# Kernel tuning notes

Measured on AMD Instinct MI355X. Metric: run time of the kernel, lower is better.

## Reference

```python
import jax, jax.numpy as jnp
import numpy as np

B, T, D, H = 4, 2048, 1024, 16
HD = D // H  # 64


def setup_inputs() -> dict:
    key = jax.random.key(0)
    k1, k2, k3 = jax.random.split(key, 3)
    x = jax.random.normal(k1, (B, T, D), dtype=jnp.float32)
    # xavier-uniform-ish scaling for stability
    W_qkv = jax.random.normal(k2, (3 * D, D), dtype=jnp.float32) * (1.0 / np.sqrt(D))
    W_proj = jax.random.normal(k3, (D, D), dtype=jnp.float32) * (1.0 / np.sqrt(D))
    b_proj = jnp.zeros((D,), dtype=jnp.float32)
    return {"x": x, "W_qkv": W_qkv, "W_proj": W_proj, "b_proj": b_proj}


def reference(x, W_qkv, W_proj, b_proj):
    Bx, Tx, C = x.shape
    qkv = x @ W_qkv.T                      # [B,T,3C]
    q, k, v = jnp.split(qkv, 3, axis=-1)
    # [B,T,C] -> [B,H,T,hd]
    def heads(t):
        return t.reshape(Bx, Tx, H, HD).transpose(0, 2, 1, 3)
    q, k, v = heads(q), heads(k), heads(v)
    scale = 1.0 / np.sqrt(HD)
    scores = jnp.einsum('bhqd,bhkd->bhqk', q, k) * scale  # [B,H,T,T]
    causal = jnp.tril(jnp.ones((Tx, Tx), dtype=bool))
    scores = jnp.where(causal, scores, jnp.finfo(scores.dtype).min)
    attn = jax.nn.softmax(scores, axis=-1)
    out = jnp.einsum('bhqk,bhkd->bhqd', attn, v)          # [B,H,T,hd]
    out = out.transpose(0, 2, 1, 3).reshape(Bx, Tx, C)    # [B,T,C]
    return out @ W_proj.T + b_proj
```

## Files before the change

kernel.cpp:

```cpp
#include <hip/hip_runtime.h>
#include <hip/hip_bf16.h>

#define B_  4
#define T_  2048
#define D_  1024
#define H_  16
#define HD_ 64
#define THREE_D (3 * D_)
#define TWO_D   (2 * D_)

typedef short s16x8 __attribute__((ext_vector_type(8)));
typedef float f32x4 __attribute__((ext_vector_type(4)));
typedef unsigned short u16;
typedef unsigned short u16x4 __attribute__((ext_vector_type(4)));
typedef unsigned int u32x2 __attribute__((ext_vector_type(2)));

static __device__ __forceinline__ s16x8 load8(const u16* p) {
    return *reinterpret_cast<const s16x8*>(p);
}
static __device__ __forceinline__ u16 f2bf(float f) {
    __hip_bfloat16 h = __float2bfloat16(f);
    return *reinterpret_cast<u16*>(&h);
}
static __device__ __forceinline__ unsigned pktrunc(float lo, float hi) {
#if __has_builtin(__builtin_amdgcn_perm)
    return __builtin_amdgcn_perm(__builtin_bit_cast(unsigned, hi),
                                 __builtin_bit_cast(unsigned, lo),
                                 0x07060302u);
#else
    return (__builtin_bit_cast(unsigned, hi) & 0xFFFF0000u) |
           (__builtin_bit_cast(unsigned, lo) >> 16);
#endif
}
static __device__ __forceinline__ float fast_exp2(float x) {
#if __has_builtin(__builtin_amdgcn_exp2f)
    return __builtin_amdgcn_exp2f(x);
#else
    float r;
    asm("v_exp_f32 %0, %1" : "=v"(r) : "v"(x));
    return r;
#endif
}

static __device__ __forceinline__ void gload_lds16(const u16* g, u16* l) {
#if __has_builtin(__builtin_amdgcn_global_load_lds)
    __builtin_amdgcn_global_load_lds(
        (__attribute__((address_space(1))) void*)g,
        (__attribute__((address_space(3))) void*)l, 16, 0, 0);
#else
    *reinterpret_cast<s16x8*>(l) = load8(g);
#endif
}

__global__ __launch_bounds__(256) void cvt3_f32_bf16(
    const float* __restrict__ a, u16* __restrict__ oa, int na,
    const float* __restrict__ bsrc, u16* __restrict__ ob, int nb,
    const float* __restrict__ c, u16* __restrict__ oc, int nc)
{
    int i = (blockIdx.x * 256 + threadIdx.x) * 4;
    const float* s; u16* d;
    if (i < na)                { s = a;    d = oa; }
    else if ((i -= na) < nb)   { s = bsrc; d = ob; }
    else if ((i -= nb) < nc)   { s = c;    d = oc; }
    else return;
    const float4 f = *reinterpret_cast<const float4*>(s + i);
    u16x4 r;
    r.x = f2bf(f.x); r.y = f2bf(f.y); r.z = f2bf(f.z); r.w = f2bf(f.w);
    *reinterpret_cast<u16x4*>(d + i) = r;
}

template<int MODE>
__global__ __launch_bounds__(256) void gemm_bt128(
    const u16* __restrict__ A,
    const u16* __restrict__ Bm,
    void* __restrict__ Cv,
    const float* __restrict__ bias,
    int M, int N, int K, int lda, int ldb, int ldc,
    float qsc, u16* __restrict__ vt)
{
    const int ntiles = N >> 7;
    const int nwg  = (M >> 7) * ntiles;
    const int cpx  = nwg >> 3;
    const int mtpc = cpx / ntiles;
    const int xcd  = (int)blockIdx.x & 7;
    const int lc   = (int)blockIdx.x >> 3;
    const int nt = lc / mtpc;
    const int mt = xcd * mtpc + (lc % mtpc);
    const int m0 = mt * 128, n0 = nt * 128;
    const int tid  = threadIdx.x;
    const int lane = tid & 63;
    const int l15  = lane & 15;
    const int quad = lane >> 4;
    const int wave = tid >> 6;
    const int wm = (wave >> 1) * 64;
    const int wn = (wave & 1) * 64;

    __shared__ u16 A_sh[2][128 * 32];
    __shared__ u16 B_sh[2][128 * 32];

    f32x4 acc[4][4] = {};

    const int c0 = tid, c1 = tid + 256;
    const int ar0 = c0 >> 2, as0 = (((c0 & 3) ^ ((c0 >> 3) & 3)) * 8);
    const int ar1 = c1 >> 2, as1 = (((c1 & 3) ^ ((c1 >> 3) & 3)) * 8);
    const u16* Ag0 = A  + (size_t)(m0 + ar0) * lda + as0;
    const u16* Ag1 = A  + (size_t)(m0 + ar1) * lda + as1;
    const u16* Bg0 = Bm + (size_t)(n0 + ar0) * ldb + as0;
    const u16* Bg1 = Bm + (size_t)(n0 + ar1) * ldb + as1;

    const int rsw2 = (l15 >> 1) & 3;
    const int rdo  = ((quad ^ rsw2) * 8);

    for (int k0 = 0; k0 < K; k0 += 64) {
        __syncthreads();
        #pragma unroll
        for (int p = 0; p < 2; ++p) {
            gload_lds16(Ag0 + k0 + p * 32, &A_sh[p][c0 * 8]);
            gload_lds16(Ag1 + k0 + p * 32, &A_sh[p][c1 * 8]);
            gload_lds16(Bg0 + k0 + p * 32, &B_sh[p][c0 * 8]);
            gload_lds16(Bg1 + k0 + p * 32, &B_sh[p][c1 * 8]);
        }
        __syncthreads();

        #pragma unroll
        for (int p = 0; p < 2; ++p) {
            s16x8 a[4], b[4];
            #pragma unroll
            for (int i = 0; i < 4; ++i) {
                a[i] = *reinterpret_cast<const s16x8*>(&A_sh[p][(wm + i * 16 + l15) * 32 + rdo]);
                b[i] = *reinterpret_cast<const s16x8*>(&B_sh[p][(wn + i * 16 + l15) * 32 + rdo]);
            }
            #pragma unroll
            for (int mi = 0; mi < 4; ++mi)
                #pragma unroll
                for (int ni = 0; ni < 4; ++ni)
                    acc[mi][ni] = __builtin_amdgcn_mfma_f32_16x16x32_bf16(
                        a[mi], b[ni], acc[mi][ni], 0, 0, 0);
        }
    }

    #pragma unroll
    for (int ni = 0; ni < 4; ++ni) {
        const int col = n0 + wn + ni * 16 + l15;
        if (MODE == 0) {
            const float bv = bias ? bias[col] : 0.0f;
            #pragma unroll
            for (int mi = 0; mi < 4; ++mi) {
                const int row = m0 + wm + mi * 16 + quad * 4;
                #pragma unroll
                for (int r = 0; r < 4; ++r)
                    ((float*)Cv)[(size_t)(row + r) * ldc + col] = acc[mi][ni][r] + bv;
            }
        } else {
            if (col < TWO_D) {
                const float sc = (col < D_) ? qsc : 1.0f;
                #pragma unroll
                for (int mi = 0; mi < 4; ++mi) {
                    const int row = m0 + wm + mi * 16 + quad * 4;
                    #pragma unroll
                    for (int r = 0; r < 4; ++r)
                        ((u16*)Cv)[(size_t)(row + r) * ldc + col] = f2bf(acc[mi][ni][r] * sc);
                }
            } else {
                const int vc = col - TWO_D;
                #pragma unroll
                for (int mi = 0; mi < 4; ++mi) {
                    const int row = m0 + wm + mi * 16 + quad * 4;
                    const int bb = row >> 11, t = row & (T_ - 1);
                    u16x4 pk;
                    #pragma unroll
                    for (int r = 0; r < 4; ++r) pk[r] = f2bf(acc[mi][ni][r]);
                    *reinterpret_cast<u16x4*>(
                        vt + ((size_t)(bb * H_ * HD_) + vc) * T_ + t) = pk;
                }
            }
        }
    }
}

__global__ __launch_bounds__(256) void flash_attn6x(
    const u16* __restrict__ qk, const u16* __restrict__ vt,
    u16* __restrict__ out)
{
    const int cls = blockIdx.x >> 6;
    const int bh  = blockIdx.x & 63;
    const int qmap[16] = {15,14,13,12, 8,9,10,11, 7,6,5,4, 0,1,2,3};
    const int qt = qmap[cls];
    const int h = bh & 15, b = bh >> 4;
    const int q0 = qt * 128;

    __shared__ u16 K_lds[64 * 64];
    __shared__ u16 V_lds[64 * 64];
    __shared__ u16 P_lds[4 * 32 * 72];

    const int tid = threadIdx.x;
    const int wave = tid >> 6, lane = tid & 63;
    const int l15 = lane & 15, quad = lane >> 4;
    u16* Pw = P_lds + wave * (32 * 72);

    const int w0 = q0 + wave * 32;

    s16x8 qf[2][2];
    #pragma unroll
    for (int mi = 0; mi < 2; ++mi) {
        const size_t rowQ = (size_t)(b * T_ + w0 + mi * 16 + l15) * TWO_D + h * HD_;
        qf[mi][0] = load8(qk + rowQ + quad * 8);
        qf[mi][1] = load8(qk + rowQ + 32 + quad * 8);
    }

    f32x4 o[2][4] = {};
    f32x4 osum[2] = {};

    s16x8 ones;
    #pragma unroll
    for (int j = 0; j < 8; ++j) ones[j] = (short)0x3F80;

    const int r0 = tid >> 3;
    const int s0 = (tid & 7) * 8;
    const int wsw = (((tid & 7) ^ (r0 & 7)) * 8);
    const u16* Kg0 = qk + (size_t)(b * T_ + r0)      * TWO_D + D_ + h * HD_ + s0;
    const u16* Kg1 = qk + (size_t)(b * T_ + r0 + 32) * TWO_D + D_ + h * HD_ + s0;
    const u16* Vg0 = vt + (size_t)(bh * HD_ + r0)      * T_ + s0;
    const u16* Vg1 = vt + (size_t)(bh * HD_ + r0 + 32) * T_ + s0;

    s16x8 pk0 = load8(Kg0);
    s16x8 pk1 = load8(Kg1);
    s16x8 pv0 = load8(Vg0);
    s16x8 pv1 = load8(Vg1);

    const int rsw = l15 & 7;

    const int nkt = 2 * qt + 2;
    for (int kt = 0; kt < nkt; ++kt) {
        const int kbase = kt * 64;
        __syncthreads();
        *reinterpret_cast<s16x8*>(&K_lds[r0 * 64 + wsw])        = pk0;
        *reinterpret_cast<s16x8*>(&K_lds[(r0 + 32) * 64 + wsw]) = pk1;
        *reinterpret_cast<s16x8*>(&V_lds[r0 * 64 + wsw])        = pv0;
        *reinterpret_cast<s16x8*>(&V_lds[(r0 + 32) * 64 + wsw]) = pv1;
        __syncthreads();

        if (kt + 1 < nkt) {
            const int nb = kbase + 64;
            pk0 = load8(Kg0 + (size_t)nb * TWO_D);
            pk1 = load8(Kg1 + (size_t)nb * TWO_D);
            pv0 = load8(Vg0 + nb);
            pv1 = load8(Vg1 + nb);
        }

        if (kbase <= w0 + 31) {
            f32x4 st[2][4];
            #pragma unroll
            for (int n = 0; n < 4; ++n) {
                const s16x8 kf0 = *reinterpret_cast<const s16x8*>(
                    &K_lds[(n * 16 + l15) * 64 + ((quad ^ rsw) * 8)]);
                const s16x8 kf1 = *reinterpret_cast<const s16x8*>(
                    &K_lds[(n * 16 + l15) * 64 + (((quad ^ 4) ^ rsw) * 8)]);
                #pragma unroll
                for (int mi = 0; mi < 2; ++mi) {
                    f32x4 t = {};
                    t = __builtin_amdgcn_mfma_f32_16x16x32_bf16(kf0, qf[mi][0], t, 0, 0, 0);
                    t = __builtin_amdgcn_mfma_f32_16x16x32_bf16(kf1, qf[mi][1], t, 0, 0, 0);
                    st[mi][n] = t;
                }
            }

            const bool diag = (kbase + 63 > w0);
            #pragma unroll
            for (int mi = 0; mi < 2; ++mi) {
                const int qr = w0 + mi * 16 + l15;
                #pragma unroll
                for (int n = 0; n < 4; ++n) {
                    const int kb = kbase + n * 16 + quad * 4;
                    float e0 = fast_exp2(st[mi][n][0]);
                    float e1 = fast_exp2(st[mi][n][1]);
                    float e2 = fast_exp2(st[mi][n][2]);
                    float e3 = fast_exp2(st[mi][n][3]);
                    if (diag) {
                        if (kb + 0 > qr) e0 = 0.0f;
                        if (kb + 1 > qr) e1 = 0.0f;
                        if (kb + 2 > qr) e2 = 0.0f;
                        if (kb + 3 > qr) e3 = 0.0f;
                    }
                    u32x2 w; w.x = pktrunc(e0, e1); w.y = pktrunc(e2, e3);
                    *reinterpret_cast<u32x2*>(
                        &Pw[(mi * 16 + l15) * 72 + n * 16 + quad * 4]) = w;
                }
            }

            #pragma unroll
            for (int ks = 0; ks < 2; ++ks) {
                s16x8 pa[2];
                #pragma unroll
                for (int mi = 0; mi < 2; ++mi) {
                    pa[mi] = *reinterpret_cast<const s16x8*>(
                        &Pw[(mi * 16 + l15) * 72 + ks * 32 + quad * 8]);
                    osum[mi] = __builtin_amdgcn_mfma_f32_16x16x32_bf16(
                        pa[mi], ones, osum[mi], 0, 0, 0);
                }
                #pragma unroll
                for (int n4 = 0; n4 < 4; ++n4) {
                    const s16x8 vb = *reinterpret_cast<const s16x8*>(
                        &V_lds[(n4 * 16 + l15) * 64 + (((ks * 4 + quad) ^ rsw) * 8)]);
                    #pragma unroll
                    for (int mi = 0; mi < 2; ++mi)
                        o[mi][n4] = __builtin_amdgcn_mfma_f32_16x16x32_bf16(
                            pa[mi], vb, o[mi][n4], 0, 0, 0);
                }
            }
        }
    }

    #pragma unroll
    for (int mi = 0; mi < 2; ++mi)
        #pragma unroll
        for (int r = 0; r < 4; ++r) {
            const float inv = 1.0f / osum[mi][r];
            const size_t rowO = (size_t)(b * T_ + w0 + mi * 16 + quad * 4 + r) * D_ + h * HD_;
            #pragma unroll
            for (int n4 = 0; n4 < 4; ++n4)
                out[rowO + n4 * 16 + l15] = f2bf(o[mi][n4][r] * inv);
        }
}

extern "C" void kernel_launch(void* const* d_in, const int* in_sizes, int n_in,
                              void* d_out, int out_size, void* d_ws, size_t ws_size,
                              hipStream_t stream)
{
    const float* x     = (const float*)d_in[0];
    const float* Wqkv  = (const float*)d_in[1];
    const float* Wproj = (const float*)d_in[2];
    const float* bproj = (const float*)d_in[3];
    float* out = (float*)d_out;

    const int M = B_ * T_;
    const float cs = 0.18033688011f;

    u16* xb    = (u16*)d_ws;
    u16* wqkvb = xb    + (size_t)M * D_;
    u16* wprob = wqkvb + (size_t)THREE_D * D_;
    u16* qk    = wprob + (size_t)D_ * D_;
    u16* vtb   = qk    + (size_t)M * TWO_D;
    u16* attn  = vtb   + (size_t)B_ * H_ * HD_ * T_;

    {
        const int na = M * D_, nb = THREE_D * D_, nc = D_ * D_;
        const int total = na + nb + nc;
        cvt3_f32_bf16<<<dim3((total / 4 + 255) / 256), 256, 0, stream>>>(
            x, xb, na, Wqkv, wqkvb, nb, Wproj, wprob, nc);
    }

    gemm_bt128<1><<<dim3((M / 128) * (THREE_D / 128)), 256, 0, stream>>>(
        xb, wqkvb, qk, nullptr, M, THREE_D, D_, D_, D_, TWO_D, cs, vtb);

    flash_attn6x<<<dim3(B_ * H_ * (T_ / 128)), 256, 0, stream>>>(qk, vtb, attn);

    gemm_bt128<0><<<dim3((M / 128) * (D_ / 128)), 256, 0, stream>>>(
        attn, wprob, out, bproj, M, D_, D_, D_, D_, D_, 1.0f, nullptr);
}
```

Measured before the change: 235.3 us.

## Replace QKV GEMM with 256x256-tile 512-thread pipelined MFMA kernel

Adds a dedicated QKV projection kernel that uses 256x256 output tiles with 8 waves. K-slices are double-buffered in LDS through direct global-to-LDS loads, and staging is interleaved across four MFMA phases with barriers and priority hints. The larger tile raises arithmetic intensity and cuts global traffic per FLOP compared with the 128x128 kernel. The cost is much higher register and LDS use per workgroup (128 KB LDS) and fewer workgroups to fill the GPU.

```diff
diff --git a/kernel.cpp b/kernel.cpp
--- a/kernel.cpp
+++ b/kernel.cpp
@@ -67,6 +67,118 @@
     u16x4 r;
     r.x = f2bf(f.x); r.y = f2bf(f.y); r.z = f2bf(f.z); r.w = f2bf(f.w);
     *reinterpret_cast<u16x4*>(d + i) = r;
+}
+
+__global__ __launch_bounds__(512, 2) void gemm256p(
+    const u16* __restrict__ A, const u16* __restrict__ Bm,
+    u16* __restrict__ Cq, u16* __restrict__ vt, float qsc)
+{
+    const int mtpc = 4;
+    const int xcd = (int)blockIdx.x & 7;
+    const int lc  = (int)blockIdx.x >> 3;
+    const int nt = lc / mtpc, mt = xcd * mtpc + (lc % mtpc);
+    const int m0 = mt << 8, n0 = nt << 8;
+
+    const int tid  = threadIdx.x;
+    const int lane = tid & 63;
+    const int l15  = lane & 15;
+    const int quad = lane >> 4;
+    const int wave = tid >> 6;
+    const int wm2  = wave >> 2;
+    const int wn4  = wave & 3;
+
+    __shared__ u16 Ash[2][2][256 * 32];
+    __shared__ u16 Bsh[2][2][256 * 32];
+
+    f32x4 acc[8][4] = {};
+
+    const int scol = (((tid & 3) ^ ((tid >> 3) & 3)) * 8);
+    const u16* Ag = A  + (size_t)(m0 + (tid >> 2)) * D_ + scol;
+    const u16* Bg = Bm + (size_t)(n0 + (tid >> 2)) * D_ + scol;
+
+    const int rdo = ((quad ^ ((l15 >> 1) & 3)) * 8);
+
+#define STG(Xg, Xsh, db, kh, kt) do {                                        \
+        const size_t off_ = (size_t)(kt) * 64 + (kh) * 32;                   \
+        gload_lds16(Xg + off_, &Xsh[db][kh][(size_t)tid * 8]);               \
+        gload_lds16(Xg + (size_t)128 * D_ + off_,                            \
+                    &Xsh[db][kh][((size_t)tid + 512) * 8]);                  \
+    } while (0)
+
+#define RD_A(d, ks, mf) (*reinterpret_cast<const s16x8*>(                    \
+        &Ash[d][ks][(wm2 * 128 + (mf) * 16 + l15) * 32 + rdo]))
+#define RD_B(d, ks, nf) (*reinterpret_cast<const s16x8*>(                    \
+        &Bsh[d][ks][(wn4 * 64 + (nf) * 16 + l15) * 32 + rdo]))
+
+#define PHASE(d, ks, mh, RELB, STGCALL, VM) do {                             \
+        s16x8 af[4];                                                         \
+        _Pragma("unroll")                                                    \
+        for (int f = 0; f < 4; ++f) {                                        \
+            af[f] = RD_A(d, ks, (mh) * 4 + f);                               \
+            if (RELB) bfr[f] = RD_B(d, ks, f);                               \
+        }                                                                    \
+        STGCALL;                                                             \
+        if (VM) asm volatile("s_waitcnt vmcnt(4)" ::: "memory");             \
+        __builtin_amdgcn_s_barrier();                                        \
+        asm volatile("s_waitcnt lgkmcnt(0)" ::: "memory");                   \
+        __builtin_amdgcn_s_setprio(1);                                       \
+        _Pragma("unroll")                                                    \
+        for (int f = 0; f < 4; ++f)                                          \
+            _Pragma("unroll")                                                \
+            for (int nf = 0; nf < 4; ++nf)                                   \
+                acc[(mh) * 4 + f][nf] =                                      \
+                    __builtin_amdgcn_mfma_f32_16x16x32_bf16(                 \
+                        af[f], bfr[nf], acc[(mh) * 4 + f][nf], 0, 0, 0);     \
+        __builtin_amdgcn_s_setprio(0);                                       \
+        __builtin_amdgcn_s_barrier();                                        \
+    } while (0)
+
+    s16x8 bfr[4];
+    STG(Ag, Ash, 0, 0, 0); STG(Bg, Bsh, 0, 0, 0);
+    STG(Ag, Ash, 0, 1, 0); STG(Bg, Bsh, 0, 1, 0);
+    asm volatile("s_waitcnt vmcnt(4)" ::: "memory");
+    __builtin_amdgcn_s_barrier();
+
+    for (int t = 0; t < 16; ++t) {
+        const int d = t & 1, dn = d ^ 1;
+        const int ts = (t + 1) & 15;
+        PHASE(d, 0, 0, 1, STG(Ag, Ash, dn, 0, ts), 0);
+        PHASE(d, 0, 1, 0, STG(Bg, Bsh, dn, 0, ts), 1);
+        PHASE(d, 1, 0, 1, STG(Ag, Ash, dn, 1, ts), 0);
+        PHASE(d, 1, 1, 0, STG(Bg, Bsh, dn, 1, ts), 1);
+    }
+    asm volatile("s_waitcnt vmcnt(0)" ::: "memory");
+#undef STG
+#undef RD_A
+#undef RD_B
+#undef PHASE
+
+    #pragma unroll
+    for (int nf = 0; nf < 4; ++nf) {
+        const int col = n0 + wn4 * 64 + nf * 16 + l15;
+        if (col < TWO_D) {
+            const float sc = (col < D_) ? qsc : 1.0f;
+            #pragma unroll
+            for (int mf = 0; mf < 8; ++mf) {
+                const int row = m0 + wm2 * 128 + mf * 16 + quad * 4;
+                #pragma unroll
+                for (int r = 0; r < 4; ++r)
+                    Cq[(size_t)(row + r) * TWO_D + col] = f2bf(acc[mf][nf][r] * sc);
+            }
+        } else {
+            const int vc = col - TWO_D;
+            #pragma unroll
+            for (int mf = 0; mf < 8; ++mf) {
+                const int row = m0 + wm2 * 128 + mf * 16 + quad * 4;
+                const int bb = row >> 11, tt = row & (T_ - 1);
+                u16x4 pk;
+                #pragma unroll
+                for (int r = 0; r < 4; ++r) pk[r] = f2bf(acc[mf][nf][r]);
+                *reinterpret_cast<u16x4*>(
+                    vt + ((size_t)(bb * H_ * HD_) + vc) * T_ + tt) = pk;
+            }
+        }
+    }
 }
 
 template<int MODE>
@@ -350,8 +462,8 @@
             x, xb, na, Wqkv, wqkvb, nb, Wproj, wprob, nc);
     }
 
-    gemm_bt128<1><<<dim3((M / 128) * (THREE_D / 128)), 256, 0, stream>>>(
-        xb, wqkvb, qk, nullptr, M, THREE_D, D_, D_, D_, TWO_D, cs, vtb);
+    gemm256p<<<dim3((M / 256) * (THREE_D / 256)), 512, 0, stream>>>(
+        xb, wqkvb, qk, vtb, cs);
 
     flash_attn6x<<<dim3(B_ * H_ * (T_ / 128)), 256, 0, stream>>>(qk, vtb, attn);
 
```

Measured after the change: 259.3 us. 1.1x slower.
